# Performance work log

Hardware: AMD Instinct MI355X
Metric: run time of the kernel (lower is better)

Reference implementation:

```python
import jax, jax.numpy as jnp
import numpy as np

N = 15000        # nodes
E = 240000       # edges (avg degree 16)
IN_DIM = 100
HID = 128
N_ETYPES = 13
N_STEPS = 6
N_GRAPHS = 64
N_CLASSES = 10


def setup_inputs() -> dict:
    key = jax.random.key(0)
    ks = jax.random.split(key, 12)
    feat = jax.random.normal(ks[0], (N, IN_DIM), dtype=jnp.float32)
    src = jax.random.randint(ks[1], (E,), 0, N, dtype=jnp.int32)
    dst = jax.random.randint(ks[2], (E,), 0, N, dtype=jnp.int32)
    etypes = jax.random.randint(ks[3], (E,), 0, N_ETYPES, dtype=jnp.int32)
    graph_ids = jnp.sort(jax.random.randint(ks[4], (N,), 0, N_GRAPHS, dtype=jnp.int32))
    s = 1.0 / np.sqrt(HID)
    W_e = jax.random.normal(ks[5], (N_ETYPES, HID, HID), dtype=jnp.float32) * s
    b_e = jax.random.normal(ks[6], (N_ETYPES, HID), dtype=jnp.float32) * s
    W_ih = jax.random.normal(ks[7], (3 * HID, HID), dtype=jnp.float32) * s
    W_hh = jax.random.normal(ks[8], (3 * HID, HID), dtype=jnp.float32) * s
    b_ih = jax.random.normal(ks[9], (3 * HID,), dtype=jnp.float32) * s
    b_hh = jax.random.normal(ks[10], (3 * HID,), dtype=jnp.float32) * s
    W_cls = jax.random.normal(ks[11], (N_CLASSES, HID), dtype=jnp.float32) * s
    b_cls = jnp.zeros((N_CLASSES,), dtype=jnp.float32)
    return {"feat": feat, "src": src, "dst": dst, "etypes": etypes,
            "graph_ids": graph_ids, "W_e": W_e, "b_e": b_e,
            "W_ih": W_ih, "W_hh": W_hh, "b_ih": b_ih, "b_hh": b_hh,
            "W_cls": W_cls, "b_cls": b_cls}


def _ggnn_forward(feat, src, dst, etypes, graph_ids, W_e, b_e, W_ih, W_hh, b_ih, b_hh, W_cls, b_cls):
    # DGL GatedGraphConv: zero-pad input features up to out_feats
    h = jnp.pad(feat, ((0, 0), (0, HID - IN_DIM)))  # [N, HID]
    for _ in range(N_STEPS):
        # per-etype linear transform of all nodes: [T, N, HID]
        Wh = jnp.einsum('nd,tdh->tnh', h, W_e) + b_e[:, None, :]
        # per-edge message = linear[etype](h[src]) via gather; scatter-sum to dst
        msg = Wh[etypes, src]                                  # [E, HID]
        a = jax.ops.segment_sum(msg, dst, num_segments=N)      # [N, HID]
        # torch GRUCell update (gate order r, z, n)
        gi = a @ W_ih.T + b_ih
        gh = h @ W_hh.T + b_hh
        ir, iz, inn = jnp.split(gi, 3, axis=-1)
        hr, hz, hn = jnp.split(gh, 3, axis=-1)
        r = jax.nn.sigmoid(ir + hr)
        z = jax.nn.sigmoid(iz + hz)
        n = jnp.tanh(inn + r * hn)
        h = (1.0 - z) * n + z * h
    # dgl.sum_nodes: sum node states per graph in the batch
    hg = jax.ops.segment_sum(h, graph_ids, num_segments=N_GRAPHS)  # [G, HID]
    return hg @ W_cls.T + b_cls                                    # [G, N_CLASSES]


def reference(feat, src, dst, etypes, graph_ids, W_e, b_e, W_ih, W_hh, b_ih, b_hh, W_cls, b_cls):
    return _ggnn_forward(feat, src, dst, etypes, graph_ids, W_e, b_e, W_ih, W_hh, b_ih, b_hh, W_cls, b_cls)
```

## Files before the change

kernel.cpp:

```cpp
#include <hip/hip_runtime.h>
#include <math.h>

#define N_NODES 15000
#define NPAD    15104
#define E_EDGES 240000
#define IN_DIM  100
#define HID     128
#define N_ETYPES 13
#define N_STEPS  6
#define N_GRAPHS 64
#define N_CLASSES 10
#define NTS     (N_ETYPES * NPAD)
#define NSB     384

typedef short v8bf __attribute__((ext_vector_type(8)));
typedef float v4f  __attribute__((ext_vector_type(4)));

union FragU { uint4 u; v8bf b; };

static __device__ __forceinline__ float bf2f(unsigned short u) {
    union { unsigned int i; float f; } x; x.i = ((unsigned int)u) << 16; return x.f;
}
static __device__ __forceinline__ unsigned short f2bf(float f) {
    union { float f; unsigned int i; } x; x.f = f;
    unsigned int u = x.i;
    u = (u + 0x7fff + ((u >> 16) & 1)) >> 16;
    return (unsigned short)u;
}
static __device__ __forceinline__ float sigm(float x) { return 1.f / (1.f + expf(-x)); }

__global__ __launch_bounds__(256) void k_initW(
    const float* __restrict__ feat,
    const float* __restrict__ W_e, const float* __restrict__ W_ih, const float* __restrict__ W_hh,
    float* __restrict__ h32, unsigned short* __restrict__ h_hi, unsigned short* __restrict__ h_lo,
    unsigned short* __restrict__ WeH,
    unsigned short* __restrict__ WihH, unsigned short* __restrict__ WhhH)
{
    int idx = blockIdx.x * 256 + threadIdx.x;
    const int IH = NPAD * HID;
    const int NE = N_ETYPES * 2048;
    const int NG = 16 * 384;
    if (idx < IH) {
        int n = idx >> 7, c = idx & 127;
        float v = 0.f;
        if (n < N_NODES && c < IN_DIM) v = feat[n * IN_DIM + c];
        h32[idx] = v;
        unsigned short hi = f2bf(v);
        h_hi[idx] = hi;
        h_lo[idx] = f2bf(v - bf2f(hi));
        return;
    }
    int f = idx - IH;
    unsigned short th[8];
    if (f < NE) {
        int t = f >> 11, r = f & 2047, kcsub = r >> 7, c = r & 127;
        #pragma unroll
        for (int j = 0; j < 8; ++j)
            th[j] = f2bf(W_e[(long)t * 16384 + (kcsub * 8 + j) * 128 + c]);
        *(uint4*)(WeH + (long)t * 16384 + ((kcsub << 7) + c) * 8) = *(uint4*)th;
    } else if (f < NE + 2 * NG) {
        int f2 = f - NE;
        const float* srcp = (f2 < NG) ? W_ih : W_hh;
        unsigned short* dh = (f2 < NG) ? WihH : WhhH;
        int g = (f2 < NG) ? f2 : f2 - NG;
        int kcsub = g / 384, c = g - kcsub * 384;
        #pragma unroll
        for (int j = 0; j < 8; ++j)
            th[j] = f2bf(srcp[(long)c * 128 + kcsub * 8 + j]);
        *(uint4*)(dh + ((long)kcsub * 384 + c) * 8) = *(uint4*)th;
    }
}

__global__ __launch_bounds__(256) void k_zero2(int* __restrict__ deg, int* __restrict__ used) {
    int idx = blockIdx.x * 256 + threadIdx.x;
    if (idx < NPAD) deg[idx] = 0;
    else if (idx < NPAD + NTS) used[idx - NPAD] = 0;
}

__global__ __launch_bounds__(256) void k_count_mark(const int* __restrict__ src,
                                                    const int* __restrict__ dst,
                                                    const int* __restrict__ et,
                                                    int* __restrict__ deg,
                                                    int* __restrict__ used) {
    int e = blockIdx.x * 256 + threadIdx.x;
    if (e >= E_EDGES) return;
    atomicAdd(&deg[dst[e]], 1);
    used[et[e] * NPAD + src[e]] = 1;
}

__global__ __launch_bounds__(1024) void k_scan(const int* __restrict__ deg,
                                               int* __restrict__ rowptr, int* __restrict__ cursor) {
    __shared__ int part[1024];
    int tid = threadIdx.x;
    const int CH = 15;
    int base = tid * CH;
    int local[CH]; int s = 0;
    #pragma unroll
    for (int i = 0; i < CH; ++i) {
        int d = (base + i < NPAD) ? deg[base + i] : 0;
        local[i] = s; s += d;
    }
    part[tid] = s; __syncthreads();
    for (int off = 1; off < 1024; off <<= 1) {
        int v = (tid >= off) ? part[tid - off] : 0;
        __syncthreads();
        part[tid] += v;
        __syncthreads();
    }
    int excl = (tid > 0) ? part[tid - 1] : 0;
    #pragma unroll
    for (int i = 0; i < CH; ++i)
        if (base + i < NPAD) { rowptr[base + i] = excl + local[i]; cursor[base + i] = excl + local[i]; }
    if (tid == 0) rowptr[NPAD] = part[1023];
}

__global__ __launch_bounds__(512) void k_su1(const int* __restrict__ used, int* __restrict__ bsum) {
    __shared__ int sh[512];
    int tid = threadIdx.x;
    int i = blockIdx.x * 512 + tid;
    sh[tid] = (i < NTS) ? used[i] : 0;
    __syncthreads();
    for (int off = 256; off > 0; off >>= 1) {
        if (tid < off) sh[tid] += sh[tid + off];
        __syncthreads();
    }
    if (tid == 0) bsum[blockIdx.x] = sh[0];
}

__global__ __launch_bounds__(512) void k_su2(const int* __restrict__ bsum, int* __restrict__ bofs) {
    __shared__ int sh[512];
    int tid = threadIdx.x;
    int v = (tid < NSB) ? bsum[tid] : 0;
    sh[tid] = v; __syncthreads();
    for (int off = 1; off < 512; off <<= 1) {
        int u = (tid >= off) ? sh[tid - off] : 0;
        __syncthreads();
        sh[tid] += u;
        __syncthreads();
    }
    if (tid < NSB) bofs[tid] = sh[tid] - v;
}

__global__ __launch_bounds__(512) void k_su3(const int* __restrict__ used,
                                             const int* __restrict__ bofs,
                                             int* __restrict__ slot,
                                             int* __restrict__ rowlist,
                                             int* __restrict__ tbase) {
    __shared__ int sh[512];
    int tid = threadIdx.x;
    int i = blockIdx.x * 512 + tid;
    int f = (i < NTS) ? used[i] : 0;
    sh[tid] = f; __syncthreads();
    for (int off = 1; off < 512; off <<= 1) {
        int u = (tid >= off) ? sh[tid - off] : 0;
        __syncthreads();
        sh[tid] += u;
        __syncthreads();
    }
    int g = bofs[blockIdx.x] + sh[tid] - f;
    if (i <= NTS) {
        if (i < NTS) slot[i] = g;
        int t = i / NPAD;
        if (i - t * NPAD == 0 || i == NTS) tbase[t] = g;
        if (f) rowlist[g] = i - t * NPAD;
    }
}

__global__ __launch_bounds__(256) void k_fill(const int* __restrict__ src, const int* __restrict__ dst,
                                              const int* __restrict__ et, const int* __restrict__ slot,
                                              int* __restrict__ cursor, int* __restrict__ eidx) {
    int e = blockIdx.x * 256 + threadIdx.x;
    if (e >= E_EDGES) return;
    int d = dst[e];
    int pos = atomicAdd(&cursor[d], 1);
    eidx[pos] = slot[et[e] * NPAD + src[e]];
}

__global__ __launch_bounds__(512) void k_egemm(
    const unsigned short* __restrict__ Ahi, const unsigned short* __restrict__ Alo,
    const uint4* __restrict__ BH,
    const float* __restrict__ bias, const int* __restrict__ tbase,
    const int* __restrict__ rowlist, unsigned short* __restrict__ C)
{
    __shared__ uint4 blds[2048];
    const int NW = 118 * N_ETYPES;
    const int q = NW / 8, r8 = NW % 8;
    int bid = blockIdx.x;
    int xcd = bid & 7, ii = bid >> 3;
    int lid = (xcd < r8 ? xcd * (q + 1) : r8 * (q + 1) + (xcd - r8) * q) + ii;
    int rg = lid / N_ETYPES, t = lid - rg * N_ETYPES;

    int base = tbase[t], end = tbase[t + 1];
    if (rg * 128 >= end - base) return;

    int tid = threadIdx.x;
    {
        const uint4* bh = BH + t * 2048;
        #pragma unroll
        for (int it = 0; it < 4; ++it) {
            int f = it * 512 + tid;
            blds[f] = bh[f];
        }
    }
    __syncthreads();

    int lane = tid & 63, w = tid >> 6;
    int gs0 = base + rg * 128 + w * 16;
    int l15 = lane & 15, lsub = lane >> 4;

    int rowslot = gs0 + l15;
    int srcrow = (rowslot < end) ? rowlist[rowslot] : 0;

    FragU ah[4], al[4];
    const char* Ahb = (const char*)Ahi;
    const char* Alb = (const char*)Alo;
    #pragma unroll
    for (int kc = 0; kc < 4; ++kc) {
        long boff = (long)srcrow * 256 + kc * 64 + lsub * 16;
        ah[kc].u = *(const uint4*)(Ahb + boff);
        al[kc].u = *(const uint4*)(Alb + boff);
    }

    v4f acc[8];
    #pragma unroll
    for (int c8 = 0; c8 < 8; ++c8) acc[c8] = (v4f)(0.f);

    #pragma unroll
    for (int kc = 0; kc < 4; ++kc)
        #pragma unroll
        for (int c8 = 0; c8 < 8; ++c8) {
            int bi = (kc * 4 + lsub) * 128 + c8 * 16 + l15;
            FragU bhf; bhf.u = blds[bi];
            acc[c8] = __builtin_amdgcn_mfma_f32_16x16x32_bf16(ah[kc].b, bhf.b, acc[c8], 0, 0, 0);
            acc[c8] = __builtin_amdgcn_mfma_f32_16x16x32_bf16(al[kc].b, bhf.b, acc[c8], 0, 0, 0);
        }

    const float* bs = bias + t * 128;
    int gbase = gs0 + lsub * 4;
    #pragma unroll
    for (int c8 = 0; c8 < 8; ++c8) {
        int col = c8 * 16 + l15;
        float bv = bs[col];
        #pragma unroll
        for (int i = 0; i < 4; ++i) {
            int gs2 = gbase + i;
            if (gs2 < end) C[(long)gs2 * 128 + col] = f2bf(acc[c8][i] + bv);
        }
    }
}

__global__ __launch_bounds__(512) void k_aggru(
    const int* __restrict__ rowptr, const int* __restrict__ eidx,
    const uint4* __restrict__ Wh,
    const uint4* __restrict__ WihH, const uint4* __restrict__ WhhH,
    const float* __restrict__ b_ih, const float* __restrict__ b_hh,
    float* __restrict__ h32,
    unsigned short* __restrict__ h_hi, unsigned short* __restrict__ h_lo)
{
    __shared__ char atile[16 * 256];
    int tid = threadIdx.x, lane = tid & 63, w = tid >> 6;
    int r0 = blockIdx.x * 16;

    {
        int g = lane >> 4, c16 = lane & 15;
        #pragma unroll
        for (int rr = 0; rr < 2; ++rr) {
            int rloc = w * 2 + rr;
            int d = r0 + rloc;
            int s = rowptr[d], e = rowptr[d + 1];
            float acc[8] = {};
            for (int i = s + g; i < e; i += 4) {
                int slot = eidx[i];
                uint4 v = Wh[(long)slot * 16 + c16];
                unsigned int ua[4] = {v.x, v.y, v.z, v.w};
                #pragma unroll
                for (int q = 0; q < 4; ++q) {
                    acc[2 * q]     += bf2f((unsigned short)(ua[q] & 0xffff));
                    acc[2 * q + 1] += bf2f((unsigned short)(ua[q] >> 16));
                }
            }
            #pragma unroll
            for (int q = 0; q < 8; ++q) {
                acc[q] += __shfl_xor(acc[q], 16);
                acc[q] += __shfl_xor(acc[q], 32);
            }
            if (g == 0) {
                unsigned short hb[8];
                #pragma unroll
                for (int q = 0; q < 8; ++q) hb[q] = f2bf(acc[q]);
                int byt = (rloc * 256 + c16 * 16) ^ ((rloc & 7) << 4);
                *(uint4*)(atile + byt) = *(uint4*)hb;
            }
        }
    }

    int cg = w;
    int l15 = lane & 15, lsub = lane >> 4;

    FragU hh[2][4];
    {
        const char* hhb = (const char*)h_hi;
        const char* hlb = (const char*)h_lo;
        #pragma unroll
        for (int kc = 0; kc < 4; ++kc) {
            long boff = (long)(r0 + l15) * 256 + kc * 64 + lsub * 16;
            hh[0][kc].u = *(const uint4*)(hhb + boff);
            hh[1][kc].u = *(const uint4*)(hlb + boff);
        }
    }
    __syncthreads();

    FragU aa[4];
    #pragma unroll
    for (int kc = 0; kc < 4; ++kc) {
        int byt = (l15 * 256 + kc * 64 + lsub * 16) ^ ((l15 & 7) << 4);
        aa[kc].u = *(const uint4*)(atile + byt);
    }

    v4f accI[3], accH[3];
    #pragma unroll
    for (int g = 0; g < 3; ++g) { accI[g] = (v4f)(0.f); accH[g] = (v4f)(0.f); }

    #pragma unroll
    for (int kc = 0; kc < 4; ++kc)
        #pragma unroll
        for (int g = 0; g < 3; ++g) {
            int bi = (kc * 4 + lsub) * 384 + g * 128 + cg * 16 + l15;
            FragU wih, whh;
            wih.u = WihH[bi]; whh.u = WhhH[bi];
            accI[g] = __builtin_amdgcn_mfma_f32_16x16x32_bf16(aa[kc].b,    wih.b, accI[g], 0, 0, 0);
            accH[g] = __builtin_amdgcn_mfma_f32_16x16x32_bf16(hh[0][kc].b, whh.b, accH[g], 0, 0, 0);
            accH[g] = __builtin_amdgcn_mfma_f32_16x16x32_bf16(hh[1][kc].b, whh.b, accH[g], 0, 0, 0);
        }

    int c = cg * 16 + l15;
    float bir = b_ih[c], biz = b_ih[c + 128], bin = b_ih[c + 256];
    float bhr = b_hh[c], bhz = b_hh[c + 128], bhn = b_hh[c + 256];
    #pragma unroll
    for (int i = 0; i < 4; ++i) {
        int row = r0 + lsub * 4 + i;
        float ir = accI[0][i] + bir, iz = accI[1][i] + biz, inn = accI[2][i] + bin;
        float hr = accH[0][i] + bhr, hz = accH[1][i] + bhz, hn = accH[2][i] + bhn;
        float rr = sigm(ir + hr);
        float zg = sigm(iz + hz);
        float ng = tanhf(inn + rr * hn);
        long off = (long)row * 128 + c;
        float ho = h32[off];
        float hv = (1.f - zg) * ng + zg * ho;
        if (row < N_NODES) {
            h32[off] = hv;
            unsigned short hi_ = f2bf(hv);
            h_hi[off] = hi_;
            h_lo[off] = f2bf(hv - bf2f(hi_));
        }
    }
}

__global__ __launch_bounds__(256) void k_pool(const float* __restrict__ h32,
                                              const int* __restrict__ gid,
                                              float* __restrict__ hg) {
    int idx = blockIdx.x * 256 + threadIdx.x;
    if (idx >= N_NODES * HID) return;
    int n = idx >> 7, c = idx & 127;
    atomicAdd(&hg[gid[n] * HID + c], h32[idx]);
}

__global__ __launch_bounds__(256) void k_zero(float* __restrict__ p, long n4) {
    long i = (long)blockIdx.x * 256 + threadIdx.x;
    if (i < n4) ((float4*)p)[i] = make_float4(0.f, 0.f, 0.f, 0.f);
}

__global__ __launch_bounds__(640) void k_cls(const float* __restrict__ hg,
                                             const float* __restrict__ Wc,
                                             const float* __restrict__ bc,
                                             float* __restrict__ out) {
    int tid = threadIdx.x;
    if (tid >= N_GRAPHS * N_CLASSES) return;
    int g = tid / N_CLASSES, c = tid - g * N_CLASSES;
    float s = bc[c];
    for (int k = 0; k < HID; ++k) s = fmaf(hg[g * HID + k], Wc[c * HID + k], s);
    out[tid] = s;
}

extern "C" void kernel_launch(void* const* d_in, const int* in_sizes, int n_in,
                              void* d_out, int out_size, void* d_ws, size_t ws_size,
                              hipStream_t stream) {
    const float* feat  = (const float*)d_in[0];
    const int*   src   = (const int*)d_in[1];
    const int*   dst   = (const int*)d_in[2];
    const int*   et    = (const int*)d_in[3];
    const int*   gid   = (const int*)d_in[4];
    const float* W_e   = (const float*)d_in[5];
    const float* b_e   = (const float*)d_in[6];
    const float* W_ih  = (const float*)d_in[7];
    const float* W_hh  = (const float*)d_in[8];
    const float* b_ih  = (const float*)d_in[9];
    const float* b_hh  = (const float*)d_in[10];
    const float* W_cls = (const float*)d_in[11];
    const float* b_cls = (const float*)d_in[12];
    float* out = (float*)d_out;

    char* p = (char*)d_ws;
    auto alloc = [&](size_t bytes) { char* r = p; p += (bytes + 255) & ~(size_t)255; return r; };
    float*          h32  = (float*)alloc((size_t)NPAD * 128 * 4);
    unsigned short* h_hi = (unsigned short*)alloc((size_t)NPAD * 128 * 2);
    unsigned short* h_lo = (unsigned short*)alloc((size_t)NPAD * 128 * 2);
    unsigned short* Wh   = (unsigned short*)alloc((size_t)NTS * 128 * 2);
    unsigned short* WeH  = (unsigned short*)alloc((size_t)N_ETYPES * 16384 * 2);
    unsigned short* WihH = (unsigned short*)alloc((size_t)16 * 384 * 8 * 2);
    unsigned short* WhhH = (unsigned short*)alloc((size_t)16 * 384 * 8 * 2);
    int* deg     = (int*)alloc((size_t)NPAD * 4);
    int* rowptr  = (int*)alloc((size_t)(NPAD + 1) * 4);
    int* cursor  = (int*)alloc((size_t)NPAD * 4);
    int* eidx    = (int*)alloc((size_t)E_EDGES * 4);
    int* used    = (int*)alloc((size_t)NTS * 4);
    int* slot    = (int*)alloc((size_t)NTS * 4);
    int* rowlist = (int*)alloc((size_t)NTS * 4);
    int* bsum    = (int*)alloc((size_t)NSB * 4);
    int* bofs    = (int*)alloc((size_t)NSB * 4);
    int* tbase   = (int*)alloc((size_t)(N_ETYPES + 1) * 4);
    float* hg    = (float*)alloc((size_t)N_GRAPHS * HID * 4);

    const int IW_GRID = (NPAD * HID + N_ETYPES * 2048 + 2 * 16 * 384 + 255) / 256;
    k_initW<<<IW_GRID, 256, 0, stream>>>(feat, W_e, W_ih, W_hh, h32, h_hi, h_lo,
                                         WeH, WihH, WhhH);
    k_zero2<<<(NPAD + NTS + 255) / 256, 256, 0, stream>>>(deg, used);
    k_count_mark<<<(E_EDGES + 255) / 256, 256, 0, stream>>>(src, dst, et, deg, used);
    k_scan<<<1, 1024, 0, stream>>>(deg, rowptr, cursor);
    k_su1<<<NSB, 512, 0, stream>>>(used, bsum);
    k_su2<<<1, 512, 0, stream>>>(bsum, bofs);
    k_su3<<<NSB, 512, 0, stream>>>(used, bofs, slot, rowlist, tbase);
    k_fill<<<(E_EDGES + 255) / 256, 256, 0, stream>>>(src, dst, et, slot, cursor, eidx);

    for (int step = 0; step < N_STEPS; ++step) {
        k_egemm<<<118 * N_ETYPES, 512, 0, stream>>>(
            h_hi, h_lo, (const uint4*)WeH, b_e, tbase, rowlist, Wh);
        k_aggru<<<NPAD / 16, 512, 0, stream>>>(
            rowptr, eidx, (const uint4*)Wh,
            (const uint4*)WihH, (const uint4*)WhhH,
            b_ih, b_hh, h32, h_hi, h_lo);
    }

    k_zero<<<(N_GRAPHS * HID / 4 + 255) / 256, 256, 0, stream>>>(hg, N_GRAPHS * HID / 4);
    k_pool<<<(N_NODES * HID + 255) / 256, 256, 0, stream>>>(h32, gid, hg);
    k_cls<<<1, 640, 0, stream>>>(hg, W_cls, b_cls, out);
}
```

Before: 475.9 us.

## Fuse setup/pool kernels, dual-accumulate edge gather, load A before B in egemm

Merges the zeroing kernels into k_initW, folds the degree scan into the used-count reduction kernel, and moves graph pooling into the last GRU step as atomics. This removes several small launches. In k_aggru the edge gather is unrolled by two with separate accumulators for more memory-level parallelism. In k_egemm the A-fragment global loads are issued before the B tile is staged to LDS, so their latency overlaps. The scan now runs in one 512-thread block with 30 elements per thread, and the pooling atomics could contend on hg.

New measurement: 486.9 us. 1.02x slower.

```diff
diff --git a/kernel.cpp b/kernel.cpp
--- a/kernel.cpp
+++ b/kernel.cpp
@@ -34,7 +34,8 @@
     const float* __restrict__ W_e, const float* __restrict__ W_ih, const float* __restrict__ W_hh,
     float* __restrict__ h32, unsigned short* __restrict__ h_hi, unsigned short* __restrict__ h_lo,
     unsigned short* __restrict__ WeH,
-    unsigned short* __restrict__ WihH, unsigned short* __restrict__ WhhH)
+    unsigned short* __restrict__ WihH, unsigned short* __restrict__ WhhH,
+    int* __restrict__ deg, int* __restrict__ used, float* __restrict__ hg)
 {
     int idx = blockIdx.x * 256 + threadIdx.x;
     const int IH = NPAD * HID;
@@ -58,23 +59,26 @@
         for (int j = 0; j < 8; ++j)
             th[j] = f2bf(W_e[(long)t * 16384 + (kcsub * 8 + j) * 128 + c]);
         *(uint4*)(WeH + (long)t * 16384 + ((kcsub << 7) + c) * 8) = *(uint4*)th;
-    } else if (f < NE + 2 * NG) {
-        int f2 = f - NE;
-        const float* srcp = (f2 < NG) ? W_ih : W_hh;
-        unsigned short* dh = (f2 < NG) ? WihH : WhhH;
-        int g = (f2 < NG) ? f2 : f2 - NG;
+        return;
+    }
+    f -= NE;
+    if (f < 2 * NG) {
+        const float* srcp = (f < NG) ? W_ih : W_hh;
+        unsigned short* dh = (f < NG) ? WihH : WhhH;
+        int g = (f < NG) ? f : f - NG;
         int kcsub = g / 384, c = g - kcsub * 384;
         #pragma unroll
         for (int j = 0; j < 8; ++j)
             th[j] = f2bf(srcp[(long)c * 128 + kcsub * 8 + j]);
         *(uint4*)(dh + ((long)kcsub * 384 + c) * 8) = *(uint4*)th;
-    }
-}
-
-__global__ __launch_bounds__(256) void k_zero2(int* __restrict__ deg, int* __restrict__ used) {
-    int idx = blockIdx.x * 256 + threadIdx.x;
-    if (idx < NPAD) deg[idx] = 0;
-    else if (idx < NPAD + NTS) used[idx - NPAD] = 0;
+        return;
+    }
+    f -= 2 * NG;
+    if (f < NPAD) { deg[f] = 0; return; }
+    f -= NPAD;
+    if (f < NTS) { used[f] = 0; return; }
+    f -= NTS;
+    if (f < N_GRAPHS * HID) hg[f] = 0.f;
 }
 
 __global__ __launch_bounds__(256) void k_count_mark(const int* __restrict__ src,
@@ -88,11 +92,25 @@
     used[et[e] * NPAD + src[e]] = 1;
 }
 
-__global__ __launch_bounds__(1024) void k_scan(const int* __restrict__ deg,
-                                               int* __restrict__ rowptr, int* __restrict__ cursor) {
-    __shared__ int part[1024];
+__global__ __launch_bounds__(512) void k_scansu1(const int* __restrict__ used,
+                                                 int* __restrict__ bsum,
+                                                 const int* __restrict__ deg,
+                                                 int* __restrict__ rowptr,
+                                                 int* __restrict__ cursor) {
+    __shared__ int sh[512];
     int tid = threadIdx.x;
-    const int CH = 15;
+    if (blockIdx.x < NSB) {
+        int i = blockIdx.x * 512 + tid;
+        sh[tid] = (i < NTS) ? used[i] : 0;
+        __syncthreads();
+        for (int off = 256; off > 0; off >>= 1) {
+            if (tid < off) sh[tid] += sh[tid + off];
+            __syncthreads();
+        }
+        if (tid == 0) bsum[blockIdx.x] = sh[0];
+        return;
+    }
+    const int CH = 30;
     int base = tid * CH;
     int local[CH]; int s = 0;
     #pragma unroll
@@ -100,31 +118,18 @@
         int d = (base + i < NPAD) ? deg[base + i] : 0;
         local[i] = s; s += d;
     }
-    part[tid] = s; __syncthreads();
-    for (int off = 1; off < 1024; off <<= 1) {
-        int v = (tid >= off) ? part[tid - off] : 0;
-        __syncthreads();
-        part[tid] += v;
-        __syncthreads();
-    }
-    int excl = (tid > 0) ? part[tid - 1] : 0;
+    sh[tid] = s; __syncthreads();
+    for (int off = 1; off < 512; off <<= 1) {
+        int v = (tid >= off) ? sh[tid - off] : 0;
+        __syncthreads();
+        sh[tid] += v;
+        __syncthreads();
+    }
+    int excl = (tid > 0) ? sh[tid - 1] : 0;
     #pragma unroll
     for (int i = 0; i < CH; ++i)
         if (base + i < NPAD) { rowptr[base + i] = excl + local[i]; cursor[base + i] = excl + local[i]; }
-    if (tid == 0) rowptr[NPAD] = part[1023];
-}
-
-__global__ __launch_bounds__(512) void k_su1(const int* __restrict__ used, int* __restrict__ bsum) {
-    __shared__ int sh[512];
-    int tid = threadIdx.x;
-    int i = blockIdx.x * 512 + tid;
-    sh[tid] = (i < NTS) ? used[i] : 0;
-    __syncthreads();
-    for (int off = 256; off > 0; off >>= 1) {
-        if (tid < off) sh[tid] += sh[tid + off];
-        __syncthreads();
-    }
-    if (tid == 0) bsum[blockIdx.x] = sh[0];
+    if (tid == 0) rowptr[NPAD] = sh[511];
 }
 
 __global__ __launch_bounds__(512) void k_su2(const int* __restrict__ bsum, int* __restrict__ bofs) {
@@ -194,16 +199,6 @@
     if (rg * 128 >= end - base) return;
 
     int tid = threadIdx.x;
-    {
-        const uint4* bh = BH + t * 2048;
-        #pragma unroll
-        for (int it = 0; it < 4; ++it) {
-            int f = it * 512 + tid;
-            blds[f] = bh[f];
-        }
-    }
-    __syncthreads();
-
     int lane = tid & 63, w = tid >> 6;
     int gs0 = base + rg * 128 + w * 16;
     int l15 = lane & 15, lsub = lane >> 4;
@@ -220,6 +215,16 @@
         ah[kc].u = *(const uint4*)(Ahb + boff);
         al[kc].u = *(const uint4*)(Alb + boff);
     }
+
+    {
+        const uint4* bh = BH + t * 2048;
+        #pragma unroll
+        for (int it = 0; it < 4; ++it) {
+            int f = it * 512 + tid;
+            blds[f] = bh[f];
+        }
+    }
+    __syncthreads();
 
     v4f acc[8];
     #pragma unroll
@@ -255,7 +260,8 @@
     const uint4* __restrict__ WihH, const uint4* __restrict__ WhhH,
     const float* __restrict__ b_ih, const float* __restrict__ b_hh,
     float* __restrict__ h32,
-    unsigned short* __restrict__ h_hi, unsigned short* __restrict__ h_lo)
+    unsigned short* __restrict__ h_hi, unsigned short* __restrict__ h_lo,
+    const int* __restrict__ gid, float* __restrict__ hg, int dopool)
 {
     __shared__ char atile[16 * 256];
     int tid = threadIdx.x, lane = tid & 63, w = tid >> 6;
@@ -269,10 +275,25 @@
             int d = r0 + rloc;
             int s = rowptr[d], e = rowptr[d + 1];
             float acc[8] = {};
-            for (int i = s + g; i < e; i += 4) {
-                int slot = eidx[i];
-                uint4 v = Wh[(long)slot * 16 + c16];
-                unsigned int ua[4] = {v.x, v.y, v.z, v.w};
+            float acc2[8] = {};
+            int i = s + g;
+            for (; i + 4 < e; i += 8) {
+                int slot0 = eidx[i], slot1 = eidx[i + 4];
+                uint4 v0 = Wh[(long)slot0 * 16 + c16];
+                uint4 v1 = Wh[(long)slot1 * 16 + c16];
+                unsigned int ua[4] = {v0.x, v0.y, v0.z, v0.w};
+                unsigned int ub[4] = {v1.x, v1.y, v1.z, v1.w};
+                #pragma unroll
+                for (int q = 0; q < 4; ++q) {
+                    acc[2 * q]      += bf2f((unsigned short)(ua[q] & 0xffff));
+                    acc[2 * q + 1]  += bf2f((unsigned short)(ua[q] >> 16));
+                    acc2[2 * q]     += bf2f((unsigned short)(ub[q] & 0xffff));
+                    acc2[2 * q + 1] += bf2f((unsigned short)(ub[q] >> 16));
+                }
+            }
+            if (i < e) {
+                uint4 v0 = Wh[(long)eidx[i] * 16 + c16];
+                unsigned int ua[4] = {v0.x, v0.y, v0.z, v0.w};
                 #pragma unroll
                 for (int q = 0; q < 4; ++q) {
                     acc[2 * q]     += bf2f((unsigned short)(ua[q] & 0xffff));
@@ -281,8 +302,10 @@
             }
             #pragma unroll
             for (int q = 0; q < 8; ++q) {
-                acc[q] += __shfl_xor(acc[q], 16);
-                acc[q] += __shfl_xor(acc[q], 32);
+                float a = acc[q] + acc2[q];
+                a += __shfl_xor(a, 16);
+                a += __shfl_xor(a, 32);
+                acc[q] = a;
             }
             if (g == 0) {
                 unsigned short hb[8];
@@ -352,22 +375,9 @@
             unsigned short hi_ = f2bf(hv);
             h_hi[off] = hi_;
             h_lo[off] = f2bf(hv - bf2f(hi_));
-        }
-    }
-}
-
-__global__ __launch_bounds__(256) void k_pool(const float* __restrict__ h32,
-                                              const int* __restrict__ gid,
-                                              float* __restrict__ hg) {
-    int idx = blockIdx.x * 256 + threadIdx.x;
-    if (idx >= N_NODES * HID) return;
-    int n = idx >> 7, c = idx & 127;
-    atomicAdd(&hg[gid[n] * HID + c], h32[idx]);
-}
-
-__global__ __launch_bounds__(256) void k_zero(float* __restrict__ p, long n4) {
-    long i = (long)blockIdx.x * 256 + threadIdx.x;
-    if (i < n4) ((float4*)p)[i] = make_float4(0.f, 0.f, 0.f, 0.f);
+            if (dopool) atomicAdd(&hg[gid[row] * HID + c], hv);
+        }
+    }
 }
 
 __global__ __launch_bounds__(640) void k_cls(const float* __restrict__ hg,
@@ -421,13 +431,12 @@
     int* tbase   = (int*)alloc((size_t)(N_ETYPES + 1) * 4);
     float* hg    = (float*)alloc((size_t)N_GRAPHS * HID * 4);
 
-    const int IW_GRID = (NPAD * HID + N_ETYPES * 2048 + 2 * 16 * 384 + 255) / 256;
+    const int IW_EXTRA = NPAD + NTS + N_GRAPHS * HID;
+    const int IW_GRID = (NPAD * HID + N_ETYPES * 2048 + 2 * 16 * 384 + IW_EXTRA + 255) / 256;
     k_initW<<<IW_GRID, 256, 0, stream>>>(feat, W_e, W_ih, W_hh, h32, h_hi, h_lo,
-                                         WeH, WihH, WhhH);
-    k_zero2<<<(NPAD + NTS + 255) / 256, 256, 0, stream>>>(deg, used);
+                                         WeH, WihH, WhhH, deg, used, hg);
     k_count_mark<<<(E_EDGES + 255) / 256, 256, 0, stream>>>(src, dst, et, deg, used);
-    k_scan<<<1, 1024, 0, stream>>>(deg, rowptr, cursor);
-    k_su1<<<NSB, 512, 0, stream>>>(used, bsum);
+    k_scansu1<<<NSB + 1, 512, 0, stream>>>(used, bsum, deg, rowptr, cursor);
     k_su2<<<1, 512, 0, stream>>>(bsum, bofs);
     k_su3<<<NSB, 512, 0, stream>>>(used, bofs, slot, rowlist, tbase);
     k_fill<<<(E_EDGES + 255) / 256, 256, 0, stream>>>(src, dst, et, slot, cursor, eidx);
@@ -438,10 +447,9 @@
         k_aggru<<<NPAD / 16, 512, 0, stream>>>(
             rowptr, eidx, (const uint4*)Wh,
             (const uint4*)WihH, (const uint4*)WhhH,
-            b_ih, b_hh, h32, h_hi, h_lo);
-    }
-
-    k_zero<<<(N_GRAPHS * HID / 4 + 255) / 256, 256, 0, stream>>>(hg, N_GRAPHS * HID / 4);
-    k_pool<<<(N_NODES * HID + 255) / 256, 256, 0, stream>>>(h32, gid, hg);
+            b_ih, b_hh, h32, h_hi, h_lo,
+            gid, hg, (step == N_STEPS - 1) ? 1 : 0);
+    }
+
     k_cls<<<1, 640, 0, stream>>>(hg, W_cls, b_cls, out);
 }
```
